# Kernel tuning notes

Hardware: AMD Instinct MI355X
Metric: run time of the kernel (lower is better)

Reference implementation:

```python
import jax, jax.numpy as jnp
import numpy as np

N = 8192   # supervoxels in current scan (queries: mean_features / ori_coords)
M = 8192   # surrounding supervoxels (keys: sur_sv_feature / sur_sv_coords)
C = 96     # feature channels
OUT = 20   # semantic classes
LG = 2048  # number of labeled supervoxels


def _pairwise_l2(x, y):
    # squared euclidean distances [n, m], clamped at 0 like torch.clamp(d, 0, inf)
    xn = jnp.sum(x * x, axis=1)[:, None]
    yn = jnp.sum(y * y, axis=1)[None, :]
    d = xn + yn - 2.0 * (x @ y.T)
    return jnp.maximum(d, 0.0)


def _cosine_distance(x1, x2, eps=1e-8):
    w1 = jnp.linalg.norm(x1, axis=1, keepdims=True)
    w2 = jnp.linalg.norm(x2, axis=1, keepdims=True)
    return 1.0 - (x1 @ x2.T) / jnp.maximum(w1 * w2.T, eps)


def setup_inputs() -> dict:
    key = jax.random.key(0)
    ks = jax.random.split(key, 8)
    sur_sv_feature = 0.05 * jax.random.normal(ks[0], (M, C), jnp.float32)
    sur_sv_coords = 0.3 * jax.random.normal(ks[1], (M, 3), jnp.float32)
    gt_idx = jax.random.randint(ks[2], (M,), 0, OUT)
    sur_sv_gt = jnp.eye(OUT, dtype=jnp.float32)[gt_idx]
    sv_prob = jax.random.normal(ks[3], (N, OUT), jnp.float32)
    mean_features = 0.05 * jax.random.normal(ks[4], (N, C), jnp.float32)
    ori_coords = 0.3 * jax.random.normal(ks[5], (N, 3), jnp.float32)
    # two near-identity invertible 4x4 pose matrices
    posses = jnp.eye(4, dtype=jnp.float32)[None, :, :] + 0.02 * jax.random.normal(ks[6], (2, 4, 4), jnp.float32)
    ran_mask = jax.random.randint(ks[7], (M,), 0, 20).astype(jnp.int32)  # torch.randint(20, ...)
    return dict(sur_sv_feature=sur_sv_feature, sur_sv_coords=sur_sv_coords,
                sur_sv_gt=sur_sv_gt, sv_prob=sv_prob, mean_features=mean_features,
                ori_coords=ori_coords, posses=posses, ran_mask=ran_mask, lg=LG)


def reference(sur_sv_feature, sur_sv_coords, sur_sv_gt, sv_prob,
              mean_features, ori_coords, posses, ran_mask, lg):
    # branch: rev=1, idx=0, sf=None
    sv_prob_sm = jax.nn.softmax(sv_prob, axis=1)
    ori_coords_in = ori_coords
    # alginment: diff = inv(posses[1]) @ posses[0]; homogeneous transform
    diff = jnp.linalg.inv(posses[1]) @ posses[0]
    homog = jnp.concatenate([sur_sv_coords,
                             jnp.ones((sur_sv_coords.shape[0], 1), sur_sv_coords.dtype)], axis=1)
    al_sur_sv_coords = (homog @ diff.T)[:, :3]

    feat_dist_cos = _cosine_distance(mean_features, sur_sv_feature)          # [N, M]
    coords_dist = _pairwise_l2(ori_coords_in, al_sur_sv_coords) / 0.25       # / 0.5**2
    sim = (1.0 + feat_dist_cos - jnp.exp(-0.5 * coords_dist)).T              # [M, N]
    sm_index = jnp.argmin(sim, axis=1)                                       # [M] nearest query per key

    onehot = sur_sv_gt
    mid_feat = mean_features[sm_index]       # [M, C]
    mid_coord = ori_coords_in[sm_index]      # [M, 3]

    upd = jnp.argmax(onehot, axis=1) < 9
    upd = upd.at[:lg].set(True)
    upd = jnp.logical_or(upd, ran_mask == 1)                                 # random refresh mask

    # masked (instead of gathered) weighted label propagation: zeroed columns
    # contribute nothing to either numerator or denominator -> same math as
    # index-selecting the update columns.
    fd = _pairwise_l2(mean_features, mid_feat)                               # [N, M]
    cd = _pairwise_l2(ori_coords_in, mid_coord) / 0.25
    dist_matric = jnp.exp(-0.5 * cd / 0.25 - 0.5 * fd / 0.09) * upd[None, :].astype(fd.dtype)
    uw = (dist_matric @ onehot) / (jnp.sum(dist_matric, axis=1, keepdims=True) + 1e-16)

    sv_prob_updated = 0.5 * sv_prob_sm + 0.5 * uw

    # re-inject labeled gt where the propagated prob agrees enough
    tmpx = jnp.argmax(onehot[:lg], axis=1)                                   # [lg]
    idx_lg = sm_index[:lg]
    vals = sv_prob_updated[idx_lg, tmpx]
    tmp = vals > 0.1
    tmp = jnp.where(jnp.any(tmp), tmp, vals > 0.0)                           # fallback threshold
    new_rows = jnp.where(tmp[:, None], onehot[:lg], sv_prob_updated[idx_lg])
    sv_prob_updated = sv_prob_updated.at[idx_lg].set(new_rows)

    maxv = jnp.max(sv_prob_updated, axis=1)
    trust9 = maxv >= 0.9
    trust = jnp.where(jnp.any(trust9), trust9, maxv >= 0.85)                 # [N] bool mask (padded form of torch.nonzero)
    pre = jnp.eye(OUT, dtype=sv_prob_updated.dtype)[jnp.argmax(sv_prob_updated, axis=1)]

    m = trust[:, None].astype(mean_features.dtype)
    return (trust, mean_features * m, ori_coords * m, pre * m,
            uw, sv_prob_updated, sm_index)
```

## Files before the change

kernel.cpp:

```cpp
#include <hip/hip_runtime.h>
#include <math.h>

#define N 8192
#define M 8192
#define C 96
#define OUT 20
#define LG 2048

#define KP2 192
#define NSPA 4
#define NSPB 4
#define LOG2E 1.4426950408889634f

typedef _Float16 h8 __attribute__((ext_vector_type(8)));
typedef float    f4 __attribute__((ext_vector_type(4)));

__device__ __forceinline__ float fexp2(float x) { return __builtin_amdgcn_exp2f(x); }

__device__ __forceinline__ void gl_lds16(const h8* g, h8* l) {
    __builtin_amdgcn_global_load_lds(
        (const __attribute__((address_space(1))) unsigned int*)g,
        (__attribute__((address_space(3))) unsigned int*)l,
        16, 0, 0);
}

__device__ __forceinline__ size_t tsm24(int row, int slot) {
    return ((size_t)(row >> 7) * 24 + slot) * 128 + (row & 127);
}

constexpr size_t OFF_AL    = 256;
constexpr size_t OFF_UPDF  = OFF_AL    + (size_t)M*3*4;
constexpr size_t OFF_GTC   = OFF_UPDF  + (size_t)M*4;
constexpr size_t OFF_SMI   = OFF_GTC   + (size_t)M*4;
constexpr size_t OFF_PERM  = OFF_SMI   + (size_t)M*4;
constexpr size_t OFF_AP    = OFF_PERM  + (size_t)M*4;
constexpr size_t OFF_BQ    = OFF_AP    + (size_t)M*KP2*2;
constexpr size_t OFF_MFP   = OFF_BQ    + (size_t)N*KP2*2;
constexpr size_t OFF_MIDH  = OFF_MFP   + (size_t)N*KP2*2;
constexpr size_t OFF_PAV   = OFF_MIDH  + (size_t)(M+256)*192;
constexpr size_t OFF_PAI   = OFF_PAV   + (size_t)NSPA*M*4;
constexpr size_t OFF_PB    = OFF_PAI   + (size_t)NSPA*M*4;
constexpr size_t OFF_POS   = OFF_PB    + (size_t)NSPB*N*OUT*4;
constexpr size_t OFF_MAXV  = OFF_POS   + (size_t)N*4;
constexpr size_t OFF_AMAX  = OFF_MAXV  + (size_t)N*4;
constexpr size_t OFF_FLAGS = OFF_AMAX  + (size_t)N*4;
constexpr size_t OFF_CNT   = OFF_FLAGS + 256;
constexpr size_t OFF_META  = OFF_CNT   + 256;
constexpr size_t OFF_NQ4   = OFF_META  + 256;
constexpr size_t OFF_SIDEQ = OFF_NQ4   + (size_t)N*16;
constexpr size_t OFF_SIDEC = OFF_SIDEQ + (size_t)(M+256)*16;

__global__ void k_prep(const float* __restrict__ ssf, const float* __restrict__ scoords,
                       const float* __restrict__ gt, const int* __restrict__ ran_mask,
                       const float* __restrict__ posses,
                       const float* __restrict__ mf, const float* __restrict__ ori,
                       float* __restrict__ al, _Float16* __restrict__ aP,
                       float* __restrict__ updf, int* __restrict__ gtcls,
                       int* __restrict__ cnt,
                       _Float16* __restrict__ bQ, _Float16* __restrict__ mfP,
                       float4* __restrict__ nq4) {
    const int tt = threadIdx.x;
    if (blockIdx.x < 256) {
        __shared__ int hcnt[OUT];
        __shared__ float sdiff[12];
        if (tt == 0) {
            float a[4][8];
            for (int i = 0; i < 4; i++)
                for (int j = 0; j < 4; j++) {
                    a[i][j]     = posses[16 + i*4 + j];
                    a[i][4 + j] = (i == j) ? 1.f : 0.f;
                }
            for (int col = 0; col < 4; col++) {
                int piv = col; float mx = fabsf(a[col][col]);
                for (int r = col + 1; r < 4; r++) {
                    float v = fabsf(a[r][col]);
                    if (v > mx) { mx = v; piv = r; }
                }
                if (piv != col)
                    for (int j = 0; j < 8; j++) { float t2 = a[col][j]; a[col][j] = a[piv][j]; a[piv][j] = t2; }
                float inv = 1.0f / a[col][col];
                for (int j = 0; j < 8; j++) a[col][j] *= inv;
                for (int r = 0; r < 4; r++) {
                    if (r == col) continue;
                    float f = a[r][col];
                    for (int j = 0; j < 8; j++) a[r][j] -= f * a[col][j];
                }
            }
            for (int i = 0; i < 3; i++)
                for (int j = 0; j < 4; j++) {
                    float s2 = 0.f;
                    for (int k = 0; k < 4; k++) s2 += a[i][4 + k] * posses[k*4 + j];
                    sdiff[i*4 + j] = s2;
                }
        }
        if (tt < OUT) hcnt[tt] = 0;
        __syncthreads();
        const int m = blockIdx.x * 32 + (tt >> 1);
        const int h = tt & 1;
        const float4* r4 = (const float4*)(ssf + (size_t)m * C);
        float4 row[12]; float s = 0.f;
        #pragma unroll
        for (int c = 0; c < 12; c++) {
            float4 v = r4[h*12 + c];
            row[c] = v;
            s += v.x*v.x + v.y*v.y + v.z*v.z + v.w*v.w;
        }
        s += __shfl_xor(s, 1, 64);
        float scale = 256.0f / sqrtf(s);
        h8* dst = (h8*)aP;
        #pragma unroll
        for (int qq = 0; qq < 6; qq++) {
            int q = h*6 + qq;
            float4 u = row[2*qq], v = row[2*qq+1];
            float xs[8] = {u.x,u.y,u.z,u.w,v.x,v.y,v.z,v.w};
            h8 hi, lo;
            #pragma unroll
            for (int e = 0; e < 8; e++) {
                float xv = xs[e] * scale;
                _Float16 hh = (_Float16)xv;
                hi[e] = hh;
                lo[e] = (_Float16)(xv - (float)hh);
            }
            dst[tsm24(m, q)]      = hi;
            dst[tsm24(m, 12 + q)] = lo;
        }
        if (h == 0) {
            float x = scoords[m*3], y = scoords[m*3+1], z = scoords[m*3+2];
            #pragma unroll
            for (int j = 0; j < 3; j++)
                al[m*3 + j] = sdiff[j*4+0]*x + sdiff[j*4+1]*y + sdiff[j*4+2]*z + sdiff[j*4+3];
            int best = 0; float bv = gt[(size_t)m*OUT];
            #pragma unroll
            for (int k = 1; k < OUT; k++) {
                float v = gt[(size_t)m*OUT + k];
                if (v > bv) { bv = v; best = k; }
            }
            gtcls[m] = best;
            bool upd = (best < 9 || m < LG || ran_mask[m] == 1);
            updf[m] = upd ? 1.f : 0.f;
            if (upd) atomicAdd(&hcnt[best], 1);
        }
        __syncthreads();
        if (tt < OUT) atomicAdd(&cnt[tt], hcnt[tt]);
    } else {
        const int n = (blockIdx.x - 256) * 32 + (tt >> 1);
        const int h = tt & 1;
        const float4* r4 = (const float4*)(mf + (size_t)n * C);
        float4 row[12]; float s = 0.f;
        #pragma unroll
        for (int c = 0; c < 12; c++) {
            float4 v = r4[h*12 + c];
            row[c] = v;
            s += v.x*v.x + v.y*v.y + v.z*v.z + v.w*v.w;
        }
        s += __shfl_xor(s, 1, 64);
        if (h == 0) {
            float4 o;
            o.x = ori[n*3]; o.y = ori[n*3+1]; o.z = ori[n*3+2]; o.w = s;
            nq4[n] = o;
        }
        float scn = 256.0f / sqrtf(s);
        h8* dB = (h8*)bQ;
        h8* dF = (h8*)mfP;
        #pragma unroll
        for (int qq = 0; qq < 6; qq++) {
            int q = h*6 + qq;
            float4 u = row[2*qq], v = row[2*qq+1];
            float xs[8] = {u.x,u.y,u.z,u.w,v.x,v.y,v.z,v.w};
            h8 hiN, loN, hiF, loF;
            #pragma unroll
            for (int e = 0; e < 8; e++) {
                float xn = xs[e] * scn;
                _Float16 hn = (_Float16)xn;
                hiN[e] = hn; loN[e] = (_Float16)(xn - (float)hn);
                float xf = xs[e] * 256.0f;
                _Float16 hf = (_Float16)xf;
                hiF[e] = hf; loF[e] = (_Float16)(xf - (float)hf);
            }
            dB[tsm24(n, q)]    = hiN;
            dB[tsm24(n, 12+q)] = loN;
            dF[tsm24(n, q)]    = hiF;
            dF[tsm24(n, 12+q)] = loF;
        }
    }
}

__global__ __launch_bounds__(1024, 1) void k_argmin(
        const _Float16* __restrict__ aP, const _Float16* __restrict__ bQ,
        const float* __restrict__ al, const float4* __restrict__ nq4,
        float* __restrict__ pav, int* __restrict__ pai) {
    __shared__ h8 sA[24*128];
    __shared__ h8 sB[2][24*128];
    __shared__ float xv[4*128];
    __shared__ int   xi[4*128];
    __shared__ float4 sMs[128];
    const int t = threadIdx.x;
    const int wave = t >> 6, lane = t & 63;
    const int col = lane & 15, quad = lane >> 4;
    const int wm = wave >> 2, wn = wave & 3;
    const int m0 = blockIdx.x * 128;
    const int sp = blockIdx.y;

    {
        const h8* gA = (const h8*)aP + (size_t)blockIdx.x * 3072;
        #pragma unroll
        for (int q = 0; q < 3; q++) gl_lds16(gA + q*1024 + t, sA + q*1024 + t);
        const h8* g = (const h8*)bQ + (size_t)sp * 3072;
        #pragma unroll
        for (int q = 0; q < 3; q++) gl_lds16(g + q*1024 + t, sB[0] + q*1024 + t);
    }
    if (t < 128) {
        float ax = al[(m0+t)*3+0], ay = al[(m0+t)*3+1], az = al[(m0+t)*3+2];
        sMs[t] = (float4){4.0f*LOG2E*ax, 4.0f*LOG2E*ay, 4.0f*LOG2E*az,
                          -2.0f*LOG2E*(ax*ax+ay*ay+az*az)};
    }
    float best[8]; int bidx[8];
    #pragma unroll
    for (int e = 0; e < 8; e++) { best[e] = 3.4e38f; bidx[e] = 0; }

    __syncthreads();

    h8 ahR[3][2], aloR[3][2];
    #pragma unroll
    for (int ks = 0; ks < 3; ks++) {
        const int hs = ks*4 + quad;
        #pragma unroll
        for (int i = 0; i < 2; i++) {
            int ml = wm*32 + i*16 + col;
            ahR[ks][i]  = sA[hs*128 + ml];
            aloR[ks][i] = sA[(12+hs)*128 + ml];
        }
    }

    const int NT = (N/128) / NSPA;
    int cur = 0;
    f4 acc[2][2];
    for (int u = 0; u < NT; u++) {
        const int tile = sp + u*NSPA;
        if (u + 1 < NT) {
            const h8* g = (const h8*)bQ + (size_t)(sp + (u+1)*NSPA) * 3072;
            #pragma unroll
            for (int q = 0; q < 3; q++) gl_lds16(g + q*1024 + t, sB[cur^1] + q*1024 + t);
        }
        #pragma unroll
        for (int i = 0; i < 2; i++)
            #pragma unroll
            for (int j = 0; j < 2; j++) acc[i][j] = (f4){0.f,0.f,0.f,0.f};

        const h8* sBc = sB[cur];
        #pragma unroll
        for (int ks = 0; ks < 3; ks++) {
            const int hs = ks*4 + quad;
            h8 bh[2], blo[2];
            #pragma unroll
            for (int j = 0; j < 2; j++) {
                int r = wn*32 + j*16 + col;
                bh[j]  = sBc[hs*128 + r];
                blo[j] = sBc[(12+hs)*128 + r];
            }
            #pragma unroll
            for (int i = 0; i < 2; i++)
                #pragma unroll
                for (int j = 0; j < 2; j++) {
                    acc[i][j] = __builtin_amdgcn_mfma_f32_16x16x32_f16(ahR[ks][i],  bh[j],  acc[i][j], 0, 0, 0);
                    acc[i][j] = __builtin_amdgcn_mfma_f32_16x16x32_f16(ahR[ks][i],  blo[j], acc[i][j], 0, 0, 0);
                    acc[i][j] = __builtin_amdgcn_mfma_f32_16x16x32_f16(aloR[ks][i], bh[j],  acc[i][j], 0, 0, 0);
                }
        }
        const int n0t = tile * 128;
        float4 o4[2]; float bn[2]; int nidx[2];
        #pragma unroll
        for (int j = 0; j < 2; j++) {
            nidx[j] = n0t + wn*32 + j*16 + col;
            o4[j] = nq4[nidx[j]];
            bn[j] = -2.0f*LOG2E*(o4[j].x*o4[j].x + o4[j].y*o4[j].y + o4[j].z*o4[j].z);
        }
        #pragma unroll
        for (int e = 0; e < 8; e++) {
            int ml = wm*32 + (e>>2)*16 + quad*4 + (e&3);
            float4 sm = sMs[ml];
            #pragma unroll
            for (int j = 0; j < 2; j++) {
                float dot = acc[e>>2][j][e&3];
                float c = sm.w + bn[j];
                c = fmaf(sm.z, o4[j].z, c);
                c = fmaf(sm.y, o4[j].y, c);
                c = fmaf(sm.x, o4[j].x, c);
                float sim = fmaf(dot, -(1.0f/65536.0f), 2.0f) - fexp2(c);
                if (sim < best[e]) { best[e] = sim; bidx[e] = nidx[j]; }
            }
        }
        __syncthreads();
        cur ^= 1;
    }
    #pragma unroll
    for (int e = 0; e < 8; e++) {
        float bv = best[e]; int bi = bidx[e];
        #pragma unroll
        for (int d = 1; d < 16; d <<= 1) {
            float ov = __shfl_xor(bv, d, 64);
            int   oi = __shfl_xor(bi, d, 64);
            if (ov < bv || (ov == bv && oi < bi)) { bv = ov; bi = oi; }
        }
        best[e] = bv; bidx[e] = bi;
    }
    if (col == 0) {
        #pragma unroll
        for (int e = 0; e < 8; e++) {
            int ml = wm*32 + (e>>2)*16 + quad*4 + (e&3);
            xv[wn*128 + ml] = best[e];
            xi[wn*128 + ml] = bidx[e];
        }
    }
    __syncthreads();
    if (t < 128) {
        float bv = xv[t]; int bi = xi[t];
        #pragma unroll
        for (int w = 1; w < 4; w++) {
            float v = xv[w*128 + t]; int i2 = xi[w*128 + t];
            if (v < bv || (v == bv && i2 < bi)) { bv = v; bi = i2; }
        }
        pav[(size_t)sp * M + m0 + t] = bv;
        pai[(size_t)sp * M + m0 + t] = bi;
    }
}

__global__ void k_scan(const int* __restrict__ cnt, int* __restrict__ meta) {
    if (threadIdx.x != 0 || blockIdx.x != 0) return;
    int run = 0;
    for (int k = 0; k < OUT; k++) { meta[2 + k] = run; run += cnt[k]; }
    meta[0] = run;
    meta[1] = (run + 255) / 256;
}

__global__ void k_permute(const float* __restrict__ pav, const int* __restrict__ pai,
                          const int* __restrict__ gtcls, const float* __restrict__ updf,
                          int* __restrict__ meta, int* __restrict__ perm,
                          int* __restrict__ smi, float* __restrict__ out_smi) {
    int m = blockIdx.x * 256 + threadIdx.x;
    if (m >= M) return;
    float best = 3.4e38f; int bidx = 0;
    for (int sp = 0; sp < NSPA; sp++) {
        float v = pav[(size_t)sp * M + m];
        int   i = pai[(size_t)sp * M + m];
        if (v < best || (v == best && i < bidx)) { best = v; bidx = i; }
    }
    smi[m] = bidx;
    out_smi[m] = (float)bidx;
    if (updf[m] == 0.f) return;
    int pos = atomicAdd(&meta[2 + gtcls[m]], 1);
    perm[pos] = m;
}

__global__ void k_gather_sorted(const int* __restrict__ meta, const int* __restrict__ perm,
                                const int* __restrict__ smi, const int* __restrict__ gtcls,
                                const _Float16* __restrict__ mfP, const float4* __restrict__ nq4,
                                _Float16* __restrict__ midH,
                                float4* __restrict__ sideQ, int* __restrict__ sideC) {
    int tid = blockIdx.x * 256 + threadIdx.x;
    int rr = tid / 12;
    int q  = tid - rr * 12;
    int mact = meta[0];
    int mpad = meta[1] * 256;
    if (rr >= mpad) return;
    h8* dst = (h8*)midH;
    size_t didx = ((size_t)(rr >> 7) * 12 + q) * 128 + (rr & 127);
    if (rr < mact) {
        int m = perm[rr];
        int s = smi[m];
        dst[didx] = ((const h8*)mfP)[tsm24(s, q)];
        if (q == 0) {
            float4 o = nq4[s];
            float4 sq;
            sq.x = o.w;
            sq.y = o.x; sq.z = o.y; sq.w = o.z;
            sideQ[rr] = sq;
            sideC[rr] = gtcls[m];
        }
    } else {
        dst[didx] = (h8)(_Float16)0.f;
        if (q == 0) {
            sideQ[rr] = (float4){1e9f, 0.f, 0.f, 0.f};
            sideC[rr] = 0;
        }
    }
}

__global__ __launch_bounds__(1024, 1) void k_uw(
        const _Float16* __restrict__ mfP, const _Float16* __restrict__ midH,
        const float4* __restrict__ nq4,
        const float4* __restrict__ sideQ, const int* __restrict__ sideC,
        const int* __restrict__ meta, float* __restrict__ pb) {
    __shared__ h8 sN[24*128];
    __shared__ h8 sB[2][2*12*128];
    __shared__ float bins[128*21];
    __shared__ float4 sSa[128];
    __shared__ float  sSb[128];
    const int t = threadIdx.x;
    const int wave = t >> 6, lane = t & 63;
    const int col = lane & 15, quad = lane >> 4;
    const int wm = wave >> 2, wn = wave & 3;
    const int n0 = blockIdx.x * 128;
    const int sp = blockIdx.y;
    const int nmac = meta[1];

    {
        const h8* gN = (const h8*)mfP + (size_t)blockIdx.x * 3072;
        #pragma unroll
        for (int q = 0; q < 3; q++) gl_lds16(gN + q*1024 + t, sN + q*1024 + t);
        if (sp < nmac) {
            const h8* g = (const h8*)midH + (size_t)(2*sp) * 1536;
            #pragma unroll
            for (int q = 0; q < 3; q++) gl_lds16(g + q*1024 + t, sB[0] + q*1024 + t);
        }
    }
    if (t < 128) {
        float4 q = nq4[n0 + t];
        sSa[t] = (float4){q.x, q.y, q.z, -8.0f*LOG2E*(q.x*q.x + q.y*q.y + q.z*q.z)};
        sSb[t] = q.w;
    }
    for (int i = t; i < 128*21; i += 1024) bins[i] = 0.f;

    __syncthreads();

    h8 ahR[3][2], aloR[3][2];
    #pragma unroll
    for (int ks = 0; ks < 3; ks++) {
        const int hs = ks*4 + quad;
        #pragma unroll
        for (int i = 0; i < 2; i++) {
            int ml = wm*32 + i*16 + col;
            ahR[ks][i]  = sN[hs*128 + ml];
            aloR[ks][i] = sN[(12+hs)*128 + ml];
        }
    }

    int cur = 0;
    f4 acc[2][4];
    for (int mt = sp; mt < nmac; mt += NSPB) {
        const int mb = mt * 256;
        if (mt + NSPB < nmac) {
            const h8* g = (const h8*)midH + (size_t)(2*(mt + NSPB)) * 1536;
            #pragma unroll
            for (int q = 0; q < 3; q++) gl_lds16(g + q*1024 + t, sB[cur^1] + q*1024 + t);
        }
        #pragma unroll
        for (int i = 0; i < 2; i++)
            #pragma unroll
            for (int j = 0; j < 4; j++) acc[i][j] = (f4){0.f,0.f,0.f,0.f};

        const h8* sBc = sB[cur];
        #pragma unroll
        for (int ks = 0; ks < 3; ks++) {
            const int hs = ks*4 + quad;
            h8 bh[4];
            #pragma unroll
            for (int j = 0; j < 4; j++) {
                int r = wn*64 + j*16 + col;
                int tb = (r >> 7) * 1536, rl = r & 127;
                bh[j]  = sBc[tb + hs*128 + rl];
            }
            #pragma unroll
            for (int i = 0; i < 2; i++)
                #pragma unroll
                for (int j = 0; j < 4; j++) {
                    acc[i][j] = __builtin_amdgcn_mfma_f32_16x16x32_f16(ahR[ks][i],  bh[j], acc[i][j], 0, 0, 0);
                    acc[i][j] = __builtin_amdgcn_mfma_f32_16x16x32_f16(aloR[ks][i], bh[j], acc[i][j], 0, 0, 0);
                }
        }
        {
            float m2[4], mx16[4], my16[4], mz16[4], bm[4]; int pc[4];
            #pragma unroll
            for (int j = 0; j < 4; j++) {
                int mm = mb + wn*64 + j*16 + col;
                float4 sq = sideQ[mm];
                m2[j] = sq.x;
                mx16[j] = 16.0f*LOG2E*sq.y; my16[j] = 16.0f*LOG2E*sq.z; mz16[j] = 16.0f*LOG2E*sq.w;
                bm[j] = -8.0f*LOG2E*(sq.y*sq.y + sq.z*sq.z + sq.w*sq.w);
                pc[j] = sideC[mm];
            }
            int seg0 = sideC[mb + wn*64];
            int seg1 = sideC[mb + wn*64 + 63];
            if (seg0 == seg1) {
                #pragma unroll
                for (int e = 0; e < 8; e++) {
                    int nl = wm*32 + (e>>2)*16 + quad*4 + (e&3);
                    float4 sa = sSa[nl];
                    float nn = sSb[nl];
                    float rs = 0.f;
                    #pragma unroll
                    for (int j = 0; j < 4; j++) {
                        float dot = acc[e>>2][j][e&3];
                        float tt = fmaf(dot, -2.0f*(1.0f/65536.0f), nn + m2[j]);
                        float fd = fmaxf(tt, 0.0f);
                        float c = sa.w + bm[j];
                        c = fmaf(sa.z, mz16[j], c);
                        c = fmaf(sa.y, my16[j], c);
                        c = fmaf(sa.x, mx16[j], c);
                        rs += fexp2(fmaf(fd, -(0.5f/0.09f)*LOG2E, c));
                    }
                    rs += __shfl_xor(rs, 1, 64);
                    rs += __shfl_xor(rs, 2, 64);
                    rs += __shfl_xor(rs, 4, 64);
                    rs += __shfl_xor(rs, 8, 64);
                    if (col == 0) atomicAdd(&bins[nl*21 + seg0], rs);
                }
            } else {
                #pragma unroll
                for (int e = 0; e < 8; e++) {
                    int nl = wm*32 + (e>>2)*16 + quad*4 + (e&3);
                    float4 sa = sSa[nl];
                    float nn = sSb[nl];
                    float w[4];
                    #pragma unroll
                    for (int j = 0; j < 4; j++) {
                        float dot = acc[e>>2][j][e&3];
                        float tt = fmaf(dot, -2.0f*(1.0f/65536.0f), nn + m2[j]);
                        float fd = fmaxf(tt, 0.0f);
                        float c = sa.w + bm[j];
                        c = fmaf(sa.z, mz16[j], c);
                        c = fmaf(sa.y, my16[j], c);
                        c = fmaf(sa.x, mx16[j], c);
                        w[j] = fexp2(fmaf(fd, -(0.5f/0.09f)*LOG2E, c));
                    }
                    for (int cc = seg0; cc <= seg1; cc++) {
                        float rs = 0.f;
                        #pragma unroll
                        for (int j = 0; j < 4; j++) rs += (pc[j] == cc) ? w[j] : 0.f;
                        rs += __shfl_xor(rs, 1, 64);
                        rs += __shfl_xor(rs, 2, 64);
                        rs += __shfl_xor(rs, 4, 64);
                        rs += __shfl_xor(rs, 8, 64);
                        if (col == 0) atomicAdd(&bins[nl*21 + cc], rs);
                    }
                }
            }
        }
        __syncthreads();
        cur ^= 1;
    }
    __syncthreads();
    for (int i = t; i < 128*OUT; i += 1024) {
        int loc = i / OUT, k = i - loc*OUT;
        pb[((size_t)sp*N + n0 + loc)*OUT + k] = bins[loc*21 + k];
    }
}

__global__ void k_uw_final(const float* __restrict__ pb, const float* __restrict__ svp,
                           float* __restrict__ out_uw, float* __restrict__ out_spu) {
    int n = blockIdx.x * 256 + threadIdx.x;
    if (n >= N) return;
    float s[OUT];
    #pragma unroll
    for (int k = 0; k < OUT; k++) s[k] = 0.f;
    for (int sp = 0; sp < NSPB; sp++) {
        size_t base = ((size_t)sp * N + n) * OUT;
        #pragma unroll
        for (int k = 0; k < OUT; k++) s[k] += pb[base + k];
    }
    float tot = 0.f;
    #pragma unroll
    for (int k = 0; k < OUT; k++) tot += s[k];
    float rden = 1.0f / (tot + 1e-16f);
    float p[OUT]; float mx = -3.4e38f;
    #pragma unroll
    for (int k = 0; k < OUT; k++) { p[k] = svp[(size_t)n*OUT + k]; mx = fmaxf(mx, p[k]); }
    float es = 0.f;
    #pragma unroll
    for (int k = 0; k < OUT; k++) { p[k] = __expf(p[k] - mx); es += p[k]; }
    float res = 1.0f / es;
    #pragma unroll
    for (int k = 0; k < OUT; k++) {
        float uw = s[k] * rden;
        out_uw[(size_t)n*OUT + k] = uw;
        out_spu[(size_t)n*OUT + k] = 0.5f * (p[k] * res) + 0.5f * uw;
    }
}

__global__ void k_scatter(const int* __restrict__ smi, const int* __restrict__ gtcls,
                          float* __restrict__ spu, int* __restrict__ pos) {
    __shared__ int sflag;
    const int t = threadIdx.x;
    if (t == 0) sflag = 0;
    __syncthreads();
    float v[2]; int idx[2];
    #pragma unroll
    for (int k = 0; k < 2; k++) {
        int i = t + k*1024;
        idx[k] = smi[i];
        v[k] = spu[(size_t)idx[k]*OUT + gtcls[i]];
        if (v[k] > 0.1f) atomicOr(&sflag, 1);
        atomicMax(&pos[idx[k]], i);
    }
    __syncthreads();
    const bool any = (sflag != 0);
    #pragma unroll
    for (int k = 0; k < 2; k++) {
        int i = t + k*1024;
        if (atomicMax(&pos[idx[k]], -1) != i) continue;
        bool tmp = any ? (v[k] > 0.1f) : (v[k] > 0.0f);
        if (!tmp) continue;
        int cls = gtcls[i];
        #pragma unroll
        for (int kk = 0; kk < OUT; kk++)
            spu[(size_t)idx[k]*OUT + kk] = (kk == cls) ? 1.0f : 0.0f;
    }
}

__global__ void k_trust_pre(const float* __restrict__ spu, float* __restrict__ maxv,
                            int* __restrict__ amax, int* __restrict__ flags) {
    int n = blockIdx.x * 256 + threadIdx.x;
    if (n >= N) return;
    float best = spu[(size_t)n*OUT]; int bi = 0;
    #pragma unroll
    for (int k = 1; k < OUT; k++) {
        float v = spu[(size_t)n*OUT + k];
        if (v > best) { best = v; bi = k; }
    }
    maxv[n] = best; amax[n] = bi;
    if (best >= 0.9f) atomicOr(&flags[1], 1);
}

__global__ void k_finalize(const float* __restrict__ mf, const float* __restrict__ ori,
                           const float* __restrict__ maxv, const int* __restrict__ amax,
                           const int* __restrict__ flags,
                           float* __restrict__ out_trust, float* __restrict__ out_mf,
                           float* __restrict__ out_ori, float* __restrict__ out_pre) {
    int n = blockIdx.x * 256 + threadIdx.x;
    if (n >= N) return;
    float mv = maxv[n];
    bool tr = flags[1] ? (mv >= 0.9f) : (mv >= 0.85f);
    float m = tr ? 1.f : 0.f;
    out_trust[n] = m;
    const float4* src = (const float4*)(mf + (size_t)n * C);
    float4* dst = (float4*)(out_mf + (size_t)n * C);
    #pragma unroll
    for (int c = 0; c < 24; c++) {
        float4 v = src[c];
        v.x *= m; v.y *= m; v.z *= m; v.w *= m;
        dst[c] = v;
    }
    out_ori[n*3]   = ori[n*3]   * m;
    out_ori[n*3+1] = ori[n*3+1] * m;
    out_ori[n*3+2] = ori[n*3+2] * m;
    int bi = amax[n];
    #pragma unroll
    for (int k = 0; k < OUT; k++) out_pre[(size_t)n*OUT + k] = (k == bi) ? m : 0.f;
}

extern "C" void kernel_launch(void* const* d_in, const int* in_sizes, int n_in,
                              void* d_out, int out_size, void* d_ws, size_t ws_size,
                              hipStream_t stream) {
    (void)in_sizes; (void)n_in; (void)out_size; (void)ws_size;
    const float* ssf     = (const float*)d_in[0];
    const float* scoords = (const float*)d_in[1];
    const float* gt      = (const float*)d_in[2];
    const float* svp     = (const float*)d_in[3];
    const float* mf      = (const float*)d_in[4];
    const float* ori     = (const float*)d_in[5];
    const float* posses  = (const float*)d_in[6];
    const int*   ran     = (const int*)d_in[7];

    float* out = (float*)d_out;
    float* out_trust = out;
    float* out_mf    = out_trust + N;
    float* out_ori   = out_mf + (size_t)N*C;
    float* out_pre   = out_ori + (size_t)N*3;
    float* out_uw    = out_pre + (size_t)N*OUT;
    float* out_spu   = out_uw  + (size_t)N*OUT;
    float* out_smi   = out_spu + (size_t)N*OUT;

    char* ws = (char*)d_ws;
    float*     w_al    = (float*)(ws + OFF_AL);
    float*     w_updf  = (float*)(ws + OFF_UPDF);
    int*       w_gtc   = (int*)(ws + OFF_GTC);
    int*       w_smi   = (int*)(ws + OFF_SMI);
    int*       w_perm  = (int*)(ws + OFF_PERM);
    _Float16*  w_aP    = (_Float16*)(ws + OFF_AP);
    _Float16*  w_bQ    = (_Float16*)(ws + OFF_BQ);
    _Float16*  w_mfP   = (_Float16*)(ws + OFF_MFP);
    _Float16*  w_midH  = (_Float16*)(ws + OFF_MIDH);
    float*     w_pav   = (float*)(ws + OFF_PAV);
    int*       w_pai   = (int*)(ws + OFF_PAI);
    float*     w_pb    = (float*)(ws + OFF_PB);
    int*       w_pos   = (int*)(ws + OFF_POS);
    float*     w_maxv  = (float*)(ws + OFF_MAXV);
    int*       w_amax  = (int*)(ws + OFF_AMAX);
    int*       w_flags = (int*)(ws + OFF_FLAGS);
    int*       w_cnt   = (int*)(ws + OFF_CNT);
    int*       w_meta  = (int*)(ws + OFF_META);
    float4*    w_nq4   = (float4*)(ws + OFF_NQ4);
    float4*    w_sideQ = (float4*)(ws + OFF_SIDEQ);
    int*       w_sideC = (int*)(ws + OFF_SIDEC);

    hipMemsetAsync(w_pos, 0xFF, (size_t)N*4, stream);
    hipMemsetAsync(w_flags, 0, 8, stream);
    hipMemsetAsync(w_cnt, 0, OUT*4, stream);

    k_prep<<<512, 64, 0, stream>>>(ssf, scoords, gt, ran, posses, mf, ori,
                                   w_al, w_aP, w_updf, w_gtc, w_cnt,
                                   w_bQ, w_mfP, w_nq4);
    k_argmin<<<dim3(M/128, NSPA), 1024, 0, stream>>>(w_aP, w_bQ, w_al, w_nq4, w_pav, w_pai);
    k_scan<<<1, 64, 0, stream>>>(w_cnt, w_meta);
    k_permute<<<M/256, 256, 0, stream>>>(w_pav, w_pai, w_gtc, w_updf, w_meta, w_perm,
                                         w_smi, out_smi);
    k_gather_sorted<<<((M+256)*12)/256, 256, 0, stream>>>(w_meta, w_perm, w_smi, w_gtc,
                                                          w_mfP, w_nq4,
                                                          w_midH, w_sideQ, w_sideC);
    k_uw<<<dim3(N/128, NSPB), 1024, 0, stream>>>(w_mfP, w_midH, w_nq4,
                                                 w_sideQ, w_sideC, w_meta, w_pb);
    k_uw_final<<<N/256, 256, 0, stream>>>(w_pb, svp, out_uw, out_spu);
    k_scatter<<<1, 1024, 0, stream>>>(w_smi, w_gtc, out_spu, w_pos);
    k_trust_pre<<<N/256, 256, 0, stream>>>(out_spu, w_maxv, w_amax, w_flags);
    k_finalize<<<N/256, 256, 0, stream>>>(mf, ori, w_maxv, w_amax, w_flags,
                                          out_trust, out_mf, out_ori, out_pre);
}
```

Baseline: 233.0 us.

## Shrink argmin and uw tiles to 64 rows with 512-thread blocks

The argmin and propagation GEMM kernels now use 64-row tiles and 512-thread blocks with launch bounds allowing four blocks per CU, in place of one 1024-thread block. This doubles the grid so more CUs stay busy and latency hides better, and the LDS loads are re-indexed to pull 64-wide slices from the existing 128-wide tiled layout. k_prep also moves to four threads per row across twice as many blocks. In exchange, each wave does less MFMA work per B-tile load, so LDS traffic rises relative to compute, and k_uw runs more reduction and atomic steps per output.

Measured after the change: 244.1 us. 1.05x slower.

```diff
diff --git a/kernel.cpp b/kernel.cpp
--- a/kernel.cpp
+++ b/kernel.cpp
@@ -60,7 +60,7 @@
                        _Float16* __restrict__ bQ, _Float16* __restrict__ mfP,
                        float4* __restrict__ nq4) {
     const int tt = threadIdx.x;
-    if (blockIdx.x < 256) {
+    if (blockIdx.x < 512) {
         __shared__ int hcnt[OUT];
         __shared__ float sdiff[12];
         if (tt == 0) {
@@ -95,22 +95,23 @@
         }
         if (tt < OUT) hcnt[tt] = 0;
         __syncthreads();
-        const int m = blockIdx.x * 32 + (tt >> 1);
-        const int h = tt & 1;
+        const int m = blockIdx.x * 16 + (tt >> 2);
+        const int h = tt & 3;
         const float4* r4 = (const float4*)(ssf + (size_t)m * C);
-        float4 row[12]; float s = 0.f;
-        #pragma unroll
-        for (int c = 0; c < 12; c++) {
-            float4 v = r4[h*12 + c];
+        float4 row[6]; float s = 0.f;
+        #pragma unroll
+        for (int c = 0; c < 6; c++) {
+            float4 v = r4[h*6 + c];
             row[c] = v;
             s += v.x*v.x + v.y*v.y + v.z*v.z + v.w*v.w;
         }
         s += __shfl_xor(s, 1, 64);
+        s += __shfl_xor(s, 2, 64);
         float scale = 256.0f / sqrtf(s);
         h8* dst = (h8*)aP;
         #pragma unroll
-        for (int qq = 0; qq < 6; qq++) {
-            int q = h*6 + qq;
+        for (int qq = 0; qq < 3; qq++) {
+            int q = h*3 + qq;
             float4 u = row[2*qq], v = row[2*qq+1];
             float xs[8] = {u.x,u.y,u.z,u.w,v.x,v.y,v.z,v.w};
             h8 hi, lo;
@@ -143,17 +144,18 @@
         __syncthreads();
         if (tt < OUT) atomicAdd(&cnt[tt], hcnt[tt]);
     } else {
-        const int n = (blockIdx.x - 256) * 32 + (tt >> 1);
-        const int h = tt & 1;
+        const int n = (blockIdx.x - 512) * 16 + (tt >> 2);
+        const int h = tt & 3;
         const float4* r4 = (const float4*)(mf + (size_t)n * C);
-        float4 row[12]; float s = 0.f;
-        #pragma unroll
-        for (int c = 0; c < 12; c++) {
-            float4 v = r4[h*12 + c];
+        float4 row[6]; float s = 0.f;
+        #pragma unroll
+        for (int c = 0; c < 6; c++) {
+            float4 v = r4[h*6 + c];
             row[c] = v;
             s += v.x*v.x + v.y*v.y + v.z*v.z + v.w*v.w;
         }
         s += __shfl_xor(s, 1, 64);
+        s += __shfl_xor(s, 2, 64);
         if (h == 0) {
             float4 o;
             o.x = ori[n*3]; o.y = ori[n*3+1]; o.z = ori[n*3+2]; o.w = s;
@@ -163,8 +165,8 @@
         h8* dB = (h8*)bQ;
         h8* dF = (h8*)mfP;
         #pragma unroll
-        for (int qq = 0; qq < 6; qq++) {
-            int q = h*6 + qq;
+        for (int qq = 0; qq < 3; qq++) {
+            int q = h*3 + qq;
             float4 u = row[2*qq], v = row[2*qq+1];
             float xs[8] = {u.x,u.y,u.z,u.w,v.x,v.y,v.z,v.w};
             h8 hiN, loN, hiF, loF;
@@ -185,31 +187,39 @@
     }
 }
 
-__global__ __launch_bounds__(1024, 1) void k_argmin(
+__global__ __launch_bounds__(512, 4) void k_argmin(
         const _Float16* __restrict__ aP, const _Float16* __restrict__ bQ,
         const float* __restrict__ al, const float4* __restrict__ nq4,
         float* __restrict__ pav, int* __restrict__ pai) {
-    __shared__ h8 sA[24*128];
-    __shared__ h8 sB[2][24*128];
-    __shared__ float xv[4*128];
-    __shared__ int   xi[4*128];
-    __shared__ float4 sMs[128];
+    __shared__ h8 sA[24*64];
+    __shared__ h8 sB[2][24*64];
+    __shared__ float xv[4*64];
+    __shared__ int   xi[4*64];
+    __shared__ float4 sMs[64];
     const int t = threadIdx.x;
     const int wave = t >> 6, lane = t & 63;
     const int col = lane & 15, quad = lane >> 4;
     const int wm = wave >> 2, wn = wave & 3;
-    const int m0 = blockIdx.x * 128;
+    const int m0 = blockIdx.x * 64;
     const int sp = blockIdx.y;
 
     {
-        const h8* gA = (const h8*)aP + (size_t)blockIdx.x * 3072;
-        #pragma unroll
-        for (int q = 0; q < 3; q++) gl_lds16(gA + q*1024 + t, sA + q*1024 + t);
-        const h8* g = (const h8*)bQ + (size_t)sp * 3072;
-        #pragma unroll
-        for (int q = 0; q < 3; q++) gl_lds16(g + q*1024 + t, sB[0] + q*1024 + t);
-    }
-    if (t < 128) {
+        const h8* gA = (const h8*)aP + (size_t)(m0 >> 7) * 3072 + (m0 & 127);
+        #pragma unroll
+        for (int q = 0; q < 3; q++) {
+            int idx = q*512 + t;
+            int slot = idx >> 6, off = idx & 63;
+            gl_lds16(gA + slot*128 + off, sA + idx);
+        }
+        const h8* g = (const h8*)bQ + (size_t)(sp >> 1) * 3072 + (sp & 1) * 64;
+        #pragma unroll
+        for (int q = 0; q < 3; q++) {
+            int idx = q*512 + t;
+            int slot = idx >> 6, off = idx & 63;
+            gl_lds16(g + slot*128 + off, sB[0] + idx);
+        }
+    }
+    if (t < 64) {
         float ax = al[(m0+t)*3+0], ay = al[(m0+t)*3+1], az = al[(m0+t)*3+2];
         sMs[t] = (float4){4.0f*LOG2E*ax, 4.0f*LOG2E*ay, 4.0f*LOG2E*az,
                           -2.0f*LOG2E*(ax*ax+ay*ay+az*az)};
@@ -227,68 +237,57 @@
         #pragma unroll
         for (int i = 0; i < 2; i++) {
             int ml = wm*32 + i*16 + col;
-            ahR[ks][i]  = sA[hs*128 + ml];
-            aloR[ks][i] = sA[(12+hs)*128 + ml];
-        }
-    }
-
-    const int NT = (N/128) / NSPA;
+            ahR[ks][i]  = sA[hs*64 + ml];
+            aloR[ks][i] = sA[(12+hs)*64 + ml];
+        }
+    }
+
+    const int NT = (N/64) / NSPA;
     int cur = 0;
-    f4 acc[2][2];
+    f4 acc[2];
     for (int u = 0; u < NT; u++) {
         const int tile = sp + u*NSPA;
         if (u + 1 < NT) {
-            const h8* g = (const h8*)bQ + (size_t)(sp + (u+1)*NSPA) * 3072;
-            #pragma unroll
-            for (int q = 0; q < 3; q++) gl_lds16(g + q*1024 + t, sB[cur^1] + q*1024 + t);
-        }
-        #pragma unroll
-        for (int i = 0; i < 2; i++)
-            #pragma unroll
-            for (int j = 0; j < 2; j++) acc[i][j] = (f4){0.f,0.f,0.f,0.f};
+            const int t2 = sp + (u+1)*NSPA;
+            const h8* g = (const h8*)bQ + (size_t)(t2 >> 1) * 3072 + (t2 & 1) * 64;
+            #pragma unroll
+            for (int q = 0; q < 3; q++) {
+                int idx = q*512 + t;
+                int slot = idx >> 6, off = idx & 63;
+                gl_lds16(g + slot*128 + off, sB[cur^1] + idx);
+            }
+        }
+        acc[0] = (f4){0.f,0.f,0.f,0.f};
+        acc[1] = (f4){0.f,0.f,0.f,0.f};
 
         const h8* sBc = sB[cur];
         #pragma unroll
         for (int ks = 0; ks < 3; ks++) {
             const int hs = ks*4 + quad;
-            h8 bh[2], blo[2];
-            #pragma unroll
-            for (int j = 0; j < 2; j++) {
-                int r = wn*32 + j*16 + col;
-                bh[j]  = sBc[hs*128 + r];
-                blo[j] = sBc[(12+hs)*128 + r];
-            }
-            #pragma unroll
-            for (int i = 0; i < 2; i++)
-                #pragma unroll
-                for (int j = 0; j < 2; j++) {
-                    acc[i][j] = __builtin_amdgcn_mfma_f32_16x16x32_f16(ahR[ks][i],  bh[j],  acc[i][j], 0, 0, 0);
-                    acc[i][j] = __builtin_amdgcn_mfma_f32_16x16x32_f16(ahR[ks][i],  blo[j], acc[i][j], 0, 0, 0);
-                    acc[i][j] = __builtin_amdgcn_mfma_f32_16x16x32_f16(aloR[ks][i], bh[j],  acc[i][j], 0, 0, 0);
-                }
-        }
-        const int n0t = tile * 128;
-        float4 o4[2]; float bn[2]; int nidx[2];
-        #pragma unroll
-        for (int j = 0; j < 2; j++) {
-            nidx[j] = n0t + wn*32 + j*16 + col;
-            o4[j] = nq4[nidx[j]];
-            bn[j] = -2.0f*LOG2E*(o4[j].x*o4[j].x + o4[j].y*o4[j].y + o4[j].z*o4[j].z);
-        }
+            const int r = wn*16 + col;
+            h8 bh  = sBc[hs*64 + r];
+            h8 blo = sBc[(12+hs)*64 + r];
+            #pragma unroll
+            for (int i = 0; i < 2; i++) {
+                acc[i] = __builtin_amdgcn_mfma_f32_16x16x32_f16(ahR[ks][i],  bh,  acc[i], 0, 0, 0);
+                acc[i] = __builtin_amdgcn_mfma_f32_16x16x32_f16(ahR[ks][i],  blo, acc[i], 0, 0, 0);
+                acc[i] = __builtin_amdgcn_mfma_f32_16x16x32_f16(aloR[ks][i], bh,  acc[i], 0, 0, 0);
+            }
+        }
+        const int n = tile*64 + wn*16 + col;
+        float4 o = nq4[n];
+        float bn = -2.0f*LOG2E*(o.x*o.x + o.y*o.y + o.z*o.z);
         #pragma unroll
         for (int e = 0; e < 8; e++) {
             int ml = wm*32 + (e>>2)*16 + quad*4 + (e&3);
             float4 sm = sMs[ml];
-            #pragma unroll
-            for (int j = 0; j < 2; j++) {
-                float dot = acc[e>>2][j][e&3];
-                float c = sm.w + bn[j];
-                c = fmaf(sm.z, o4[j].z, c);
-                c = fmaf(sm.y, o4[j].y, c);
-                c = fmaf(sm.x, o4[j].x, c);
-                float sim = fmaf(dot, -(1.0f/65536.0f), 2.0f) - fexp2(c);
-                if (sim < best[e]) { best[e] = sim; bidx[e] = nidx[j]; }
-            }
+            float dot = acc[e>>2][e&3];
+            float c = sm.w + bn;
+            c = fmaf(sm.z, o.z, c);
+            c = fmaf(sm.y, o.y, c);
+            c = fmaf(sm.x, o.x, c);
+            float sim = fmaf(dot, -(1.0f/65536.0f), 2.0f) - fexp2(c);
+            if (sim < best[e]) { best[e] = sim; bidx[e] = n; }
         }
         __syncthreads();
         cur ^= 1;
@@ -308,16 +307,16 @@
         #pragma unroll
         for (int e = 0; e < 8; e++) {
             int ml = wm*32 + (e>>2)*16 + quad*4 + (e&3);
-            xv[wn*128 + ml] = best[e];
-            xi[wn*128 + ml] = bidx[e];
+            xv[wn*64 + ml] = best[e];
+            xi[wn*64 + ml] = bidx[e];
         }
     }
     __syncthreads();
-    if (t < 128) {
+    if (t < 64) {
         float bv = xv[t]; int bi = xi[t];
         #pragma unroll
         for (int w = 1; w < 4; w++) {
-            float v = xv[w*128 + t]; int i2 = xi[w*128 + t];
+            float v = xv[w*64 + t]; int i2 = xi[w*64 + t];
             if (v < bv || (v == bv && i2 < bi)) { bv = v; bi = i2; }
         }
         pav[(size_t)sp * M + m0 + t] = bv;
@@ -386,40 +385,44 @@
     }
 }
 
-__global__ __launch_bounds__(1024, 1) void k_uw(
+__global__ __launch_bounds__(512, 4) void k_uw(
         const _Float16* __restrict__ mfP, const _Float16* __restrict__ midH,
         const float4* __restrict__ nq4,
         const float4* __restrict__ sideQ, const int* __restrict__ sideC,
         const int* __restrict__ meta, float* __restrict__ pb) {
-    __shared__ h8 sN[24*128];
-    __shared__ h8 sB[2][2*12*128];
-    __shared__ float bins[128*21];
-    __shared__ float4 sSa[128];
-    __shared__ float  sSb[128];
+    __shared__ h8 sN[24*64];
+    __shared__ h8 sB[2][12*128];
+    __shared__ float bins[64*21];
+    __shared__ float4 sSa[64];
+    __shared__ float  sSb[64];
     const int t = threadIdx.x;
     const int wave = t >> 6, lane = t & 63;
     const int col = lane & 15, quad = lane >> 4;
     const int wm = wave >> 2, wn = wave & 3;
-    const int n0 = blockIdx.x * 128;
+    const int n0 = blockIdx.x * 64;
     const int sp = blockIdx.y;
-    const int nmac = meta[1];
+    const int nmac2 = meta[1] * 2;
 
     {
-        const h8* gN = (const h8*)mfP + (size_t)blockIdx.x * 3072;
-        #pragma unroll
-        for (int q = 0; q < 3; q++) gl_lds16(gN + q*1024 + t, sN + q*1024 + t);
-        if (sp < nmac) {
-            const h8* g = (const h8*)midH + (size_t)(2*sp) * 1536;
-            #pragma unroll
-            for (int q = 0; q < 3; q++) gl_lds16(g + q*1024 + t, sB[0] + q*1024 + t);
-        }
-    }
-    if (t < 128) {
+        const h8* gN = (const h8*)mfP + (size_t)(n0 >> 7) * 3072 + (n0 & 127);
+        #pragma unroll
+        for (int q = 0; q < 3; q++) {
+            int idx = q*512 + t;
+            int slot = idx >> 6, off = idx & 63;
+            gl_lds16(gN + slot*128 + off, sN + idx);
+        }
+        if (sp < nmac2) {
+            const h8* g = (const h8*)midH + (size_t)sp * 1536;
+            #pragma unroll
+            for (int q = 0; q < 3; q++) gl_lds16(g + q*512 + t, sB[0] + q*512 + t);
+        }
+    }
+    if (t < 64) {
         float4 q = nq4[n0 + t];
         sSa[t] = (float4){q.x, q.y, q.z, -8.0f*LOG2E*(q.x*q.x + q.y*q.y + q.z*q.z)};
         sSb[t] = q.w;
     }
-    for (int i = t; i < 128*21; i += 1024) bins[i] = 0.f;
+    for (int i = t; i < 64*21; i += 512) bins[i] = 0.f;
 
     __syncthreads();
 
@@ -430,57 +433,56 @@
         #pragma unroll
         for (int i = 0; i < 2; i++) {
             int ml = wm*32 + i*16 + col;
-            ahR[ks][i]  = sN[hs*128 + ml];
-            aloR[ks][i] = sN[(12+hs)*128 + ml];
+            ahR[ks][i]  = sN[hs*64 + ml];
+            aloR[ks][i] = sN[(12+hs)*64 + ml];
         }
     }
 
     int cur = 0;
-    f4 acc[2][4];
-    for (int mt = sp; mt < nmac; mt += NSPB) {
-        const int mb = mt * 256;
-        if (mt + NSPB < nmac) {
-            const h8* g = (const h8*)midH + (size_t)(2*(mt + NSPB)) * 1536;
-            #pragma unroll
-            for (int q = 0; q < 3; q++) gl_lds16(g + q*1024 + t, sB[cur^1] + q*1024 + t);
+    f4 acc[2][2];
+    for (int mt = sp; mt < nmac2; mt += NSPB) {
+        const int mb = mt * 128;
+        if (mt + NSPB < nmac2) {
+            const h8* g = (const h8*)midH + (size_t)(mt + NSPB) * 1536;
+            #pragma unroll
+            for (int q = 0; q < 3; q++) gl_lds16(g + q*512 + t, sB[cur^1] + q*512 + t);
         }
         #pragma unroll
         for (int i = 0; i < 2; i++)
             #pragma unroll
-            for (int j = 0; j < 4; j++) acc[i][j] = (f4){0.f,0.f,0.f,0.f};
+            for (int j = 0; j < 2; j++) acc[i][j] = (f4){0.f,0.f,0.f,0.f};
 
         const h8* sBc = sB[cur];
         #pragma unroll
         for (int ks = 0; ks < 3; ks++) {
             const int hs = ks*4 + quad;
-            h8 bh[4];
-            #pragma unroll
-            for (int j = 0; j < 4; j++) {
-                int r = wn*64 + j*16 + col;
-                int tb = (r >> 7) * 1536, rl = r & 127;
-                bh[j]  = sBc[tb + hs*128 + rl];
+            h8 bh[2];
+            #pragma unroll
+            for (int j = 0; j < 2; j++) {
+                int r = wn*32 + j*16 + col;
+                bh[j] = sBc[hs*128 + r];
             }
             #pragma unroll
             for (int i = 0; i < 2; i++)
                 #pragma unroll
-                for (int j = 0; j < 4; j++) {
+                for (int j = 0; j < 2; j++) {
                     acc[i][j] = __builtin_amdgcn_mfma_f32_16x16x32_f16(ahR[ks][i],  bh[j], acc[i][j], 0, 0, 0);
                     acc[i][j] = __builtin_amdgcn_mfma_f32_16x16x32_f16(aloR[ks][i], bh[j], acc[i][j], 0, 0, 0);
                 }
         }
         {
-            float m2[4], mx16[4], my16[4], mz16[4], bm[4]; int pc[4];
-            #pragma unroll
-            for (int j = 0; j < 4; j++) {
-                int mm = mb + wn*64 + j*16 + col;
+            float m2[2], mx16[2], my16[2], mz16[2], bm[2]; int pc[2];
+            #pragma unroll
+            for (int j = 0; j < 2; j++) {
+                int mm = mb + wn*32 + j*16 + col;
                 float4 sq = sideQ[mm];
                 m2[j] = sq.x;
                 mx16[j] = 16.0f*LOG2E*sq.y; my16[j] = 16.0f*LOG2E*sq.z; mz16[j] = 16.0f*LOG2E*sq.w;
                 bm[j] = -8.0f*LOG2E*(sq.y*sq.y + sq.z*sq.z + sq.w*sq.w);
                 pc[j] = sideC[mm];
             }
-            int seg0 = sideC[mb + wn*64];
-            int seg1 = sideC[mb + wn*64 + 63];
+            int seg0 = sideC[mb + wn*32];
+            int seg1 = sideC[mb + wn*32 + 31];
             if (seg0 == seg1) {
                 #pragma unroll
                 for (int e = 0; e < 8; e++) {
@@ -489,7 +491,7 @@
                     float nn = sSb[nl];
                     float rs = 0.f;
                     #pragma unroll
-                    for (int j = 0; j < 4; j++) {
+                    for (int j = 0; j < 2; j++) {
                         float dot = acc[e>>2][j][e&3];
                         float tt = fmaf(dot, -2.0f*(1.0f/65536.0f), nn + m2[j]);
                         float fd = fmaxf(tt, 0.0f);
@@ -511,9 +513,9 @@
                     int nl = wm*32 + (e>>2)*16 + quad*4 + (e&3);
                     float4 sa = sSa[nl];
                     float nn = sSb[nl];
-                    float w[4];
+                    float w[2];
                     #pragma unroll
-                    for (int j = 0; j < 4; j++) {
+                    for (int j = 0; j < 2; j++) {
                         float dot = acc[e>>2][j][e&3];
                         float tt = fmaf(dot, -2.0f*(1.0f/65536.0f), nn + m2[j]);
                         float fd = fmaxf(tt, 0.0f);
@@ -526,7 +528,7 @@
                     for (int cc = seg0; cc <= seg1; cc++) {
                         float rs = 0.f;
                         #pragma unroll
-                        for (int j = 0; j < 4; j++) rs += (pc[j] == cc) ? w[j] : 0.f;
+                        for (int j = 0; j < 2; j++) rs += (pc[j] == cc) ? w[j] : 0.f;
                         rs += __shfl_xor(rs, 1, 64);
                         rs += __shfl_xor(rs, 2, 64);
                         rs += __shfl_xor(rs, 4, 64);
@@ -540,7 +542,7 @@
         cur ^= 1;
     }
     __syncthreads();
-    for (int i = t; i < 128*OUT; i += 1024) {
+    for (int i = t; i < 64*OUT; i += 512) {
         int loc = i / OUT, k = i - loc*OUT;
         pb[((size_t)sp*N + n0 + loc)*OUT + k] = bins[loc*21 + k];
     }
@@ -697,18 +699,18 @@
     hipMemsetAsync(w_flags, 0, 8, stream);
     hipMemsetAsync(w_cnt, 0, OUT*4, stream);
 
-    k_prep<<<512, 64, 0, stream>>>(ssf, scoords, gt, ran, posses, mf, ori,
-                                   w_al, w_aP, w_updf, w_gtc, w_cnt,
-                                   w_bQ, w_mfP, w_nq4);
-    k_argmin<<<dim3(M/128, NSPA), 1024, 0, stream>>>(w_aP, w_bQ, w_al, w_nq4, w_pav, w_pai);
+    k_prep<<<1024, 64, 0, stream>>>(ssf, scoords, gt, ran, posses, mf, ori,
+                                    w_al, w_aP, w_updf, w_gtc, w_cnt,
+                                    w_bQ, w_mfP, w_nq4);
+    k_argmin<<<dim3(M/64, NSPA), 512, 0, stream>>>(w_aP, w_bQ, w_al, w_nq4, w_pav, w_pai);
     k_scan<<<1, 64, 0, stream>>>(w_cnt, w_meta);
     k_permute<<<M/256, 256, 0, stream>>>(w_pav, w_pai, w_gtc, w_updf, w_meta, w_perm,
                                          w_smi, out_smi);
     k_gather_sorted<<<((M+256)*12)/256, 256, 0, stream>>>(w_meta, w_perm, w_smi, w_gtc,
                                                           w_mfP, w_nq4,
                                                           w_midH, w_sideQ, w_sideC);
-    k_uw<<<dim3(N/128, NSPB), 1024, 0, stream>>>(w_mfP, w_midH, w_nq4,
-                                                 w_sideQ, w_sideC, w_meta, w_pb);
+    k_uw<<<dim3(N/64, NSPB), 512, 0, stream>>>(w_mfP, w_midH, w_nq4,
+                                               w_sideQ, w_sideC, w_meta, w_pb);
     k_uw_final<<<N/256, 256, 0, stream>>>(w_pb, svp, out_uw, out_spu);
     k_scatter<<<1, 1024, 0, stream>>>(w_smi, w_gtc, out_spu, w_pos);
     k_trust_pre<<<N/256, 256, 0, stream>>>(out_spu, w_maxv, w_amax, w_flags);
```
